# Kernel optimization log

Hardware: AMD Instinct MI355X
Metric: run time of the kernel (lower is better)

The kernel has to match this reference:

```python
import jax, jax.numpy as jnp
import numpy as np

B, T, D = 4, 8192, 1024
BLOCKS, TOPK, MACRO, SLOTS = 64, 16, 4, 64
RMS_EPS = 1.1920929e-07  # torch.finfo(float32).eps, F.rms_norm default


def setup_inputs() -> dict:
    key = jax.random.key(0)
    ks = jax.random.split(key, 7)
    return {
        "prev_hidden": jax.random.normal(ks[0], (B, T, D), jnp.float32),
        "prev_nll": jax.random.uniform(ks[1], (B, T), jnp.float32),
        "query": jax.random.normal(ks[2], (SLOTS, D), jnp.float32) * 0.02,
        "W_sum": jax.random.normal(ks[3], (D, 2 * D), jnp.float32) / np.sqrt(2 * D),
        "W_k": jax.random.normal(ks[4], (D, D), jnp.float32) / np.sqrt(D),
        "W_v": jax.random.normal(ks[5], (D, D), jnp.float32) / np.sqrt(D),
        "W_o": jax.random.normal(ks[6], (D, D), jnp.float32) / np.sqrt(D),
    }


def _rms_norm(x):
    return x * jax.lax.rsqrt(jnp.mean(x * x, axis=-1, keepdims=True) + RMS_EPS)


def _zscore(x):
    m = x.mean(axis=1, keepdims=True)
    s = jnp.maximum(x.std(axis=1, keepdims=True), 1e-6)  # unbiased=False
    return (x - m) / s


def reference(prev_hidden, prev_nll, query, W_sum, W_k, W_v, W_o):
    b, t, d = prev_hidden.shape
    # --- micro segments: equal blocks (t divisible by BLOCKS -> linspace edges exact)
    L = t // BLOCKS
    seg = prev_hidden.reshape(b, BLOCKS, L, d)
    seg_mean = seg.mean(axis=2)          # [B, BLOCKS, D]
    seg_last = seg[:, :, -1, :]          # [B, BLOCKS, D]
    hid_score = jnp.linalg.norm(seg_mean, axis=-1)            # [B, BLOCKS]
    sur_score = prev_nll.reshape(b, BLOCKS, L).mean(axis=-1)  # [B, BLOCKS]
    scores = _zscore(hid_score) + _zscore(sur_score)          # utility_source='both'
    idx = jnp.sort(jax.lax.top_k(scores, TOPK)[1], axis=-1)   # [B, TOPK]
    gmean = jnp.take_along_axis(seg_mean, idx[:, :, None], axis=1)
    glast = jnp.take_along_axis(seg_last, idx[:, :, None], axis=1)
    micro = jnp.concatenate([gmean, glast], axis=-1)          # [B, TOPK, 2D]
    # --- hierarchical: macro segments + global
    Lm = t // MACRO
    mseg = prev_hidden.reshape(b, MACRO, Lm, d)
    macro = jnp.concatenate([mseg.mean(axis=2), mseg[:, :, -1, :]], axis=-1)
    glob = jnp.concatenate([prev_hidden.mean(axis=1), prev_hidden[:, -1, :]], axis=-1)[:, None, :]
    feats = jnp.concatenate([micro, macro, glob], axis=1)     # [B, S=21, 2D]
    summaries = _rms_norm(jnp.einsum('bsf,df->bsd', feats, W_sum))
    # --- cross-attention of learned prefix queries over sources
    keys = jnp.einsum('bsd,ed->bse', summaries, W_k)
    vals = jnp.einsum('bsd,ed->bse', summaries, W_v)
    logits = jnp.einsum('qd,bsd->bqs', query, keys) / jnp.sqrt(jnp.float32(d))
    attn = jax.nn.softmax(logits.astype(jnp.float32), axis=-1).astype(summaries.dtype)
    prefix = jnp.einsum('bqs,bse->bqe', attn, vals)
    return jnp.einsum('bqe,oe->bqo', prefix, W_o)
```

## Files before the change

kernel.cpp:

```cpp
#include <hip/hip_runtime.h>
#include <stdint.h>
#include <stddef.h>

#define B_ 4
#define T_ 8192
#define D_ 1024
#define NBLK 64
#define SEGL 128
#define TOPK_ 16
#define NS 21
#define MPAD 96
#define RMS_EPS_ 1.1920929e-07f

typedef float f32x4 __attribute__((ext_vector_type(4)));
typedef __bf16 bf16x8 __attribute__((ext_vector_type(8)));
typedef unsigned short us8 __attribute__((ext_vector_type(8)));

__device__ __forceinline__ unsigned short f2bf(float f) {
    union { float f; unsigned int u; } v; v.f = f;
    unsigned int r = v.u + 0x7FFFu + ((v.u >> 16) & 1u);
    return (unsigned short)(r >> 16);
}
__device__ __forceinline__ float4 ld4(const float* p) { return *(const float4*)p; }

__global__ __launch_bounds__(512) void seg_stats(
        const float* __restrict__ ph, const float* __restrict__ nll,
        float* __restrict__ seg_mean, float* __restrict__ hid, float* __restrict__ sur) {
    int g = blockIdx.x; int b = g >> 6; int blk = g & 63;
    int tid = threadIdx.x; int half = tid >> 8; int c = tid & 255;
    const float* base = ph + ((size_t)b * T_ + blk * SEGL + half * 64) * D_ + 4 * c;
    float ax = 0.f, ay = 0.f, az = 0.f, aw = 0.f;
    #pragma unroll 8
    for (int r = 0; r < 64; r++) {
        float4 v = ld4(base + (size_t)r * D_);
        ax += v.x; ay += v.y; az += v.z; aw += v.w;
    }
    __shared__ float4 tmp[256];
    __shared__ float red[256];
    __shared__ float nl[128];
    if (tid < 128) nl[tid] = nll[b * T_ + blk * SEGL + tid];
    if (half) { float4 t; t.x = ax; t.y = ay; t.z = az; t.w = aw; tmp[c] = t; }
    __syncthreads();
    if (!half) {
        float4 t2 = tmp[c];
        float mx = (ax + t2.x) * (1.f/128.f), my = (ay + t2.y) * (1.f/128.f);
        float mz = (az + t2.z) * (1.f/128.f), mw = (aw + t2.w) * (1.f/128.f);
        float4 m; m.x = mx; m.y = my; m.z = mz; m.w = mw;
        *(float4*)(seg_mean + (size_t)g * D_ + 4 * c) = m;
        red[c] = mx*mx + my*my + mz*mz + mw*mw;
    }
    __syncthreads();
    for (int s2 = 128; s2 > 0; s2 >>= 1) { if (tid < s2) red[tid] += red[tid + s2]; __syncthreads(); }
    for (int s2 = 64;  s2 > 0; s2 >>= 1) { if (tid < s2) nl[tid]  += nl[tid + s2];  __syncthreads(); }
    if (tid == 0) { hid[g] = sqrtf(red[0]); sur[g] = nl[0] * (1.f/128.f); }
}

__global__ __launch_bounds__(64) void score_topk(
        const float* __restrict__ hid, const float* __restrict__ sur, int* __restrict__ idx) {
    int b = blockIdx.x; int l = threadIdx.x;
    float h = hid[b * NBLK + l];
    float s = sur[b * NBLK + l];
    float mh = h; for (int o = 32; o; o >>= 1) mh += __shfl_xor(mh, o); mh *= (1.f/64.f);
    float dh = h - mh; float vh = dh * dh;
    for (int o = 32; o; o >>= 1) vh += __shfl_xor(vh, o); vh *= (1.f/64.f);
    float sh = fmaxf(sqrtf(vh), 1e-6f);
    float ms = s; for (int o = 32; o; o >>= 1) ms += __shfl_xor(ms, o); ms *= (1.f/64.f);
    float ds = s - ms; float vs = ds * ds;
    for (int o = 32; o; o >>= 1) vs += __shfl_xor(vs, o); vs *= (1.f/64.f);
    float ss = fmaxf(sqrtf(vs), 1e-6f);
    float z = dh / sh + ds / ss;
    __shared__ float sc[64];
    sc[l] = z;
    __syncthreads();
    int rank = 0;
    for (int j = 0; j < 64; j++) {
        float oj = sc[j];
        rank += (oj > z) || (oj == z && j < l);
    }
    bool sel = rank < TOPK_;
    unsigned long long mask = __ballot(sel);
    int pos = __popcll(mask & ((1ull << l) - 1ull));
    if (sel) idx[b * TOPK_ + pos] = l;
}

__global__ __launch_bounds__(256) void feats_build(
        const float* __restrict__ ph, const float* __restrict__ seg_mean,
        const int* __restrict__ idx, unsigned short* __restrict__ feats) {
    int r = blockIdx.x; int t = threadIdx.x;
    unsigned short* row0 = feats + (size_t)r * 2048 + 4 * t;
    unsigned short* row1 = row0 + 1024;
    if (r >= B_ * NS) {
        ushort4 z; z.x = z.y = z.z = z.w = 0;
        *(ushort4*)row0 = z; *(ushort4*)row1 = z;
        return;
    }
    int b = r / NS, s = r % NS;
    float mx = 0, my = 0, mz = 0, mw = 0;
    int lastrow;
    if (s < 16) {
        int blk = idx[b * TOPK_ + s];
        float4 v = ld4(seg_mean + (size_t)(b * NBLK + blk) * D_ + 4 * t);
        mx = v.x; my = v.y; mz = v.z; mw = v.w;
        lastrow = blk * SEGL + SEGL - 1;
    } else if (s < 20) {
        int m = s - 16;
        for (int j = 0; j < 16; j++) {
            float4 v = ld4(seg_mean + (size_t)(b * NBLK + m * 16 + j) * D_ + 4 * t);
            mx += v.x; my += v.y; mz += v.z; mw += v.w;
        }
        mx *= (1.f/16.f); my *= (1.f/16.f); mz *= (1.f/16.f); mw *= (1.f/16.f);
        lastrow = m * 2048 + 2047;
    } else {
        for (int j = 0; j < 64; j++) {
            float4 v = ld4(seg_mean + (size_t)(b * NBLK + j) * D_ + 4 * t);
            mx += v.x; my += v.y; mz += v.z; mw += v.w;
        }
        mx *= (1.f/64.f); my *= (1.f/64.f); mz *= (1.f/64.f); mw *= (1.f/64.f);
        lastrow = T_ - 1;
    }
    float4 lv = ld4(ph + ((size_t)b * T_ + lastrow) * D_ + 4 * t);
    ushort4 hm; hm.x = f2bf(mx); hm.y = f2bf(my); hm.z = f2bf(mz); hm.w = f2bf(mw);
    ushort4 hl; hl.x = f2bf(lv.x); hl.y = f2bf(lv.y); hl.z = f2bf(lv.z); hl.w = f2bf(lv.w);
    *(ushort4*)row0 = hm;
    *(ushort4*)row1 = hl;
}

template<int K>
__global__ __launch_bounds__(256) void gemm_bt2(
        const unsigned short* __restrict__ A, const float* __restrict__ Bw,
        float* __restrict__ Cf, unsigned short* __restrict__ Cb) {
    constexpr int KW = K / 4;
    constexpr int NSTEP = KW / 32;
    int n0 = blockIdx.x * 16;
    int m0 = blockIdx.y * 48;
    int tid = threadIdx.x, wave = tid >> 6, lane = tid & 63;
    int quad = lane >> 4, l16 = lane & 15;
    int kbase = wave * KW;

    f32x4 acc[3];
    #pragma unroll
    for (int i = 0; i < 3; i++) acc[i] = (f32x4){0.f, 0.f, 0.f, 0.f};

    const float* bp = Bw + (size_t)(n0 + l16) * K + kbase + quad * 8;
    const unsigned short* ap = A + (size_t)(m0 + l16) * K + kbase + quad * 8;

    #pragma unroll 4
    for (int s = 0; s < NSTEP; s++) {
        float4 b0 = ld4(bp + s * 32);
        float4 b1 = ld4(bp + s * 32 + 4);
        us8 braw;
        braw[0] = f2bf(b0.x); braw[1] = f2bf(b0.y); braw[2] = f2bf(b0.z); braw[3] = f2bf(b0.w);
        braw[4] = f2bf(b1.x); braw[5] = f2bf(b1.y); braw[6] = f2bf(b1.z); braw[7] = f2bf(b1.w);
        bf16x8 bf = __builtin_bit_cast(bf16x8, braw);
        #pragma unroll
        for (int mi = 0; mi < 3; mi++) {
            us8 araw = *(const us8*)(ap + (size_t)mi * 16 * K + s * 32);
            bf16x8 af = __builtin_bit_cast(bf16x8, araw);
            acc[mi] = __builtin_amdgcn_mfma_f32_16x16x32_bf16(af, bf, acc[mi], 0, 0, 0);
        }
    }

    __shared__ float part[4][3][16][16];
    #pragma unroll
    for (int mi = 0; mi < 3; mi++)
        #pragma unroll
        for (int r = 0; r < 4; r++)
            part[wave][mi][quad * 4 + r][l16] = acc[mi][r];
    __syncthreads();
    for (int o = tid; o < 768; o += 256) {
        int mi = o >> 8; int rr = (o >> 4) & 15; int cc = o & 15;
        float v = part[0][mi][rr][cc] + part[1][mi][rr][cc]
                + part[2][mi][rr][cc] + part[3][mi][rr][cc];
        int row = m0 + mi * 16 + rr; int col = n0 + cc;
        Cf[(size_t)row * 1024 + col] = v;
        Cb[(size_t)row * 1024 + col] = f2bf(v);
    }
}

__global__ __launch_bounds__(256) void rmsnorm_rows(
        const float* __restrict__ x, unsigned short* __restrict__ y) {
    int r = blockIdx.x; int t = threadIdx.x;
    float4 v = ld4(x + (size_t)r * D_ + 4 * t);
    __shared__ float red[256];
    red[t] = v.x*v.x + v.y*v.y + v.z*v.z + v.w*v.w;
    __syncthreads();
    for (int s2 = 128; s2 > 0; s2 >>= 1) { if (t < s2) red[t] += red[t + s2]; __syncthreads(); }
    float scale = rsqrtf(red[0] * (1.f/1024.f) + RMS_EPS_);
    ushort4 h;
    h.x = f2bf(v.x * scale); h.y = f2bf(v.y * scale);
    h.z = f2bf(v.z * scale); h.w = f2bf(v.w * scale);
    *(ushort4*)(y + (size_t)r * D_ + 4 * t) = h;
}

__global__ __launch_bounds__(256) void attn_out(
        const float* __restrict__ query, const float* __restrict__ keys,
        const float* __restrict__ valsO, float* __restrict__ out) {
    int g = blockIdx.x; int b = g >> 6; int q = g & 63;
    int tid = threadIdx.x, wave = tid >> 6, lane = tid & 63;
    __shared__ float attnw[24];
    const float* qrow = query + (size_t)q * D_ + lane * 16;
    float4 qv0 = ld4(qrow), qv1 = ld4(qrow + 4), qv2 = ld4(qrow + 8), qv3 = ld4(qrow + 12);
    for (int s = wave; s < NS; s += 4) {
        const float* krow = keys + (size_t)(b * NS + s) * D_ + lane * 16;
        float4 k0 = ld4(krow), k1 = ld4(krow + 4), k2 = ld4(krow + 8), k3 = ld4(krow + 12);
        float a = qv0.x*k0.x + qv0.y*k0.y + qv0.z*k0.z + qv0.w*k0.w
                + qv1.x*k1.x + qv1.y*k1.y + qv1.z*k1.z + qv1.w*k1.w
                + qv2.x*k2.x + qv2.y*k2.y + qv2.z*k2.z + qv2.w*k2.w
                + qv3.x*k3.x + qv3.y*k3.y + qv3.z*k3.z + qv3.w*k3.w;
        for (int o = 32; o; o >>= 1) a += __shfl_xor(a, o);
        if (lane == 0) attnw[s] = a * 0.03125f;
    }
    __syncthreads();
    if (tid == 0) {
        float mx = -1e30f;
        for (int s = 0; s < NS; s++) mx = fmaxf(mx, attnw[s]);
        float sum = 0.f;
        for (int s = 0; s < NS; s++) { float e = expf(attnw[s] - mx); attnw[s] = e; sum += e; }
        float inv = 1.f / sum;
        for (int s = 0; s < NS; s++) attnw[s] *= inv;
    }
    __syncthreads();
    float ax = 0, ay = 0, az = 0, aw = 0;
    #pragma unroll
    for (int s = 0; s < NS; s++) {
        float w = attnw[s];
        float4 v = ld4(valsO + (size_t)(b * NS + s) * D_ + 4 * tid);
        ax += w * v.x; ay += w * v.y; az += w * v.z; aw += w * v.w;
    }
    float4 o4; o4.x = ax; o4.y = ay; o4.z = az; o4.w = aw;
    *(float4*)(out + (size_t)g * D_ + 4 * tid) = o4;
}

extern "C" void kernel_launch(void* const* d_in, const int* in_sizes, int n_in,
                              void* d_out, int out_size, void* d_ws, size_t ws_size,
                              hipStream_t stream) {
    (void)in_sizes; (void)n_in; (void)out_size; (void)ws_size;
    const float* ph    = (const float*)d_in[0];
    const float* nll   = (const float*)d_in[1];
    const float* query = (const float*)d_in[2];
    const float* W_sum = (const float*)d_in[3];
    const float* W_k   = (const float*)d_in[4];
    const float* W_v   = (const float*)d_in[5];
    const float* W_o   = (const float*)d_in[6];
    float* out = (float*)d_out;

    char* ws = (char*)d_ws;
    float*          seg_mean = (float*)(ws + 0);
    float*          hid      = (float*)(ws + 1048576);
    float*          sur      = (float*)(ws + 1049600);
    int*            idx      = (int*)  (ws + 1050624);
    unsigned short* feats    = (unsigned short*)(ws + 1050880);
    float*          presum_f = (float*)(ws + 1444096);
    unsigned short* presum_b = (unsigned short*)(ws + 1837312);
    unsigned short* summ_b   = (unsigned short*)(ws + 2033920);
    float*          keys_f   = (float*)(ws + 2230528);
    unsigned short* keys_b   = (unsigned short*)(ws + 2623744);
    float*          vals_f   = (float*)(ws + 2820352);
    unsigned short* vals_b   = (unsigned short*)(ws + 3213568);
    float*          valsO_f  = (float*)(ws + 3410176);
    unsigned short* valsO_b  = (unsigned short*)(ws + 3803392);

    seg_stats<<<B_ * NBLK, 512, 0, stream>>>(ph, nll, seg_mean, hid, sur);
    score_topk<<<B_, 64, 0, stream>>>(hid, sur, idx);
    feats_build<<<MPAD, 256, 0, stream>>>(ph, seg_mean, idx, feats);
    gemm_bt2<2048><<<dim3(64, 2), 256, 0, stream>>>(feats, W_sum, presum_f, presum_b);
    rmsnorm_rows<<<MPAD, 256, 0, stream>>>(presum_f, summ_b);
    gemm_bt2<1024><<<dim3(64, 2), 256, 0, stream>>>(summ_b, W_k, keys_f, keys_b);
    gemm_bt2<1024><<<dim3(64, 2), 256, 0, stream>>>(summ_b, W_v, vals_f, vals_b);
    gemm_bt2<1024><<<dim3(64, 2), 256, 0, stream>>>(vals_b, W_o, valsO_f, valsO_b);
    attn_out<<<B_ * NBLK, 256, 0, stream>>>(query, keys_f, valsO_f, out);
}
```

Before: 261.5 us.

## Fuse top-k into feats build, RMSnorm into GEMM, batch K/V projections

Folds the score/top-k kernel into feats_build, so each block recomputes the z-scores and ranks for its batch. The RMS sum of squares now comes from the W_sum GEMM epilogue via atomics, and the scale is applied while loading A in the next GEMM, which removes the rmsnorm kernel. The W_k and W_v GEMMs become a single launch that uses blockIdx.y to pick the weight. The GEMM changes from 4 to 8 waves with all 96 rows per block, and unused bf16/fp32 outputs are dropped. This removes several launches and intermediate buffers, at the cost of a memset, atomics, redundant top-k work per block, and fp32 A loads with on-the-fly conversion.

```diff
diff --git a/kernel.cpp b/kernel.cpp
--- a/kernel.cpp
+++ b/kernel.cpp
@@ -55,50 +55,53 @@
     if (tid == 0) { hid[g] = sqrtf(red[0]); sur[g] = nl[0] * (1.f/128.f); }
 }
 
-__global__ __launch_bounds__(64) void score_topk(
-        const float* __restrict__ hid, const float* __restrict__ sur, int* __restrict__ idx) {
-    int b = blockIdx.x; int l = threadIdx.x;
-    float h = hid[b * NBLK + l];
-    float s = sur[b * NBLK + l];
-    float mh = h; for (int o = 32; o; o >>= 1) mh += __shfl_xor(mh, o); mh *= (1.f/64.f);
-    float dh = h - mh; float vh = dh * dh;
-    for (int o = 32; o; o >>= 1) vh += __shfl_xor(vh, o); vh *= (1.f/64.f);
-    float sh = fmaxf(sqrtf(vh), 1e-6f);
-    float ms = s; for (int o = 32; o; o >>= 1) ms += __shfl_xor(ms, o); ms *= (1.f/64.f);
-    float ds = s - ms; float vs = ds * ds;
-    for (int o = 32; o; o >>= 1) vs += __shfl_xor(vs, o); vs *= (1.f/64.f);
-    float ss = fmaxf(sqrtf(vs), 1e-6f);
-    float z = dh / sh + ds / ss;
-    __shared__ float sc[64];
-    sc[l] = z;
-    __syncthreads();
-    int rank = 0;
-    for (int j = 0; j < 64; j++) {
-        float oj = sc[j];
-        rank += (oj > z) || (oj == z && j < l);
-    }
-    bool sel = rank < TOPK_;
-    unsigned long long mask = __ballot(sel);
-    int pos = __popcll(mask & ((1ull << l) - 1ull));
-    if (sel) idx[b * TOPK_ + pos] = l;
-}
-
 __global__ __launch_bounds__(256) void feats_build(
         const float* __restrict__ ph, const float* __restrict__ seg_mean,
-        const int* __restrict__ idx, unsigned short* __restrict__ feats) {
+        const float* __restrict__ hid, const float* __restrict__ sur,
+        unsigned short* __restrict__ feats) {
     int r = blockIdx.x; int t = threadIdx.x;
     unsigned short* row0 = feats + (size_t)r * 2048 + 4 * t;
     unsigned short* row1 = row0 + 1024;
     if (r >= B_ * NS) {
-        ushort4 z; z.x = z.y = z.z = z.w = 0;
-        *(ushort4*)row0 = z; *(ushort4*)row1 = z;
+        ushort4 z4; z4.x = z4.y = z4.z = z4.w = 0;
+        *(ushort4*)row0 = z4; *(ushort4*)row1 = z4;
         return;
     }
     int b = r / NS, s = r % NS;
+    __shared__ float sc[64];
+    __shared__ int sidx[16];
+    if (t < 64) {
+        float h = hid[b * NBLK + t];
+        float ss0 = sur[b * NBLK + t];
+        float mh = h; for (int o = 32; o; o >>= 1) mh += __shfl_xor(mh, o); mh *= (1.f/64.f);
+        float dh = h - mh; float vh = dh * dh;
+        for (int o = 32; o; o >>= 1) vh += __shfl_xor(vh, o); vh *= (1.f/64.f);
+        float sh = fmaxf(sqrtf(vh), 1e-6f);
+        float ms = ss0; for (int o = 32; o; o >>= 1) ms += __shfl_xor(ms, o); ms *= (1.f/64.f);
+        float ds = ss0 - ms; float vs = ds * ds;
+        for (int o = 32; o; o >>= 1) vs += __shfl_xor(vs, o); vs *= (1.f/64.f);
+        float ssd = fmaxf(sqrtf(vs), 1e-6f);
+        sc[t] = dh / sh + ds / ssd;
+    }
+    __syncthreads();
+    if (t < 64) {
+        float z = sc[t];
+        int rank = 0;
+        for (int j = 0; j < 64; j++) {
+            float oj = sc[j];
+            rank += (oj > z) || (oj == z && j < t);
+        }
+        bool sel = rank < TOPK_;
+        unsigned long long mask = __ballot(sel);
+        int pos = __popcll(mask & ((1ull << t) - 1ull));
+        if (sel) sidx[pos] = t;
+    }
+    __syncthreads();
+
     float mx = 0, my = 0, mz = 0, mw = 0;
     int lastrow;
     if (s < 16) {
-        int blk = idx[b * TOPK_ + s];
+        int blk = sidx[s];
         float4 v = ld4(seg_mean + (size_t)(b * NBLK + blk) * D_ + 4 * t);
         mx = v.x; my = v.y; mz = v.z; mw = v.w;
         lastrow = blk * SEGL + SEGL - 1;
@@ -125,24 +128,36 @@
     *(ushort4*)row1 = hl;
 }
 
-template<int K>
-__global__ __launch_bounds__(256) void gemm_bt2(
-        const unsigned short* __restrict__ A, const float* __restrict__ Bw,
-        float* __restrict__ Cf, unsigned short* __restrict__ Cb) {
-    constexpr int KW = K / 4;
+template<int K, int MODE>
+__global__ __launch_bounds__(512) void gemm_v3(
+        const void* __restrict__ Av,
+        const float* __restrict__ B0, const float* __restrict__ B1,
+        float* __restrict__ C0f, unsigned short* __restrict__ C0b,
+        float* __restrict__ C1f, unsigned short* __restrict__ C1b,
+        float* __restrict__ sumsq) {
+    constexpr int KW = K / 8;
     constexpr int NSTEP = KW / 32;
+    const float* Bw = (MODE == 2 && blockIdx.y) ? B1 : B0;
+    float* Cf          = (MODE == 2 && blockIdx.y) ? C1f : C0f;
+    unsigned short* Cb = (MODE == 2 && blockIdx.y) ? C1b : C0b;
+
     int n0 = blockIdx.x * 16;
-    int m0 = blockIdx.y * 48;
     int tid = threadIdx.x, wave = tid >> 6, lane = tid & 63;
     int quad = lane >> 4, l16 = lane & 15;
     int kbase = wave * KW;
 
-    f32x4 acc[3];
-    #pragma unroll
-    for (int i = 0; i < 3; i++) acc[i] = (f32x4){0.f, 0.f, 0.f, 0.f};
+    f32x4 acc[6];
+    #pragma unroll
+    for (int i = 0; i < 6; i++) acc[i] = (f32x4){0.f, 0.f, 0.f, 0.f};
+
+    float scl[6];
+    if (MODE == 2) {
+        #pragma unroll
+        for (int mi = 0; mi < 6; mi++)
+            scl[mi] = rsqrtf(sumsq[mi * 16 + l16] * (1.f/1024.f) + RMS_EPS_);
+    }
 
     const float* bp = Bw + (size_t)(n0 + l16) * K + kbase + quad * 8;
-    const unsigned short* ap = A + (size_t)(m0 + l16) * K + kbase + quad * 8;
 
     #pragma unroll 4
     for (int s = 0; s < NSTEP; s++) {
@@ -151,45 +166,52 @@
         us8 braw;
         braw[0] = f2bf(b0.x); braw[1] = f2bf(b0.y); braw[2] = f2bf(b0.z); braw[3] = f2bf(b0.w);
         braw[4] = f2bf(b1.x); braw[5] = f2bf(b1.y); braw[6] = f2bf(b1.z); braw[7] = f2bf(b1.w);
-        bf16x8 bf = __builtin_bit_cast(bf16x8, braw);
-        #pragma unroll
-        for (int mi = 0; mi < 3; mi++) {
-            us8 araw = *(const us8*)(ap + (size_t)mi * 16 * K + s * 32);
-            bf16x8 af = __builtin_bit_cast(bf16x8, araw);
-            acc[mi] = __builtin_amdgcn_mfma_f32_16x16x32_bf16(af, bf, acc[mi], 0, 0, 0);
-        }
-    }
-
-    __shared__ float part[4][3][16][16];
-    #pragma unroll
-    for (int mi = 0; mi < 3; mi++)
+        bf16x8 bfr = __builtin_bit_cast(bf16x8, braw);
+        #pragma unroll
+        for (int mi = 0; mi < 6; mi++) {
+            bf16x8 af;
+            if (MODE == 2) {
+                const float* apf = (const float*)Av + (size_t)(mi * 16 + l16) * K + kbase + quad * 8 + s * 32;
+                float4 a0 = ld4(apf), a1 = ld4(apf + 4);
+                us8 ar;
+                ar[0] = f2bf(a0.x * scl[mi]); ar[1] = f2bf(a0.y * scl[mi]);
+                ar[2] = f2bf(a0.z * scl[mi]); ar[3] = f2bf(a0.w * scl[mi]);
+                ar[4] = f2bf(a1.x * scl[mi]); ar[5] = f2bf(a1.y * scl[mi]);
+                ar[6] = f2bf(a1.z * scl[mi]); ar[7] = f2bf(a1.w * scl[mi]);
+                af = __builtin_bit_cast(bf16x8, ar);
+            } else {
+                af = __builtin_bit_cast(bf16x8,
+                    *(const us8*)((const unsigned short*)Av + (size_t)(mi * 16 + l16) * K + kbase + quad * 8 + s * 32));
+            }
+            acc[mi] = __builtin_amdgcn_mfma_f32_16x16x32_bf16(af, bfr, acc[mi], 0, 0, 0);
+        }
+    }
+
+    __shared__ float part[8][6][16][16];
+    #pragma unroll
+    for (int mi = 0; mi < 6; mi++)
         #pragma unroll
         for (int r = 0; r < 4; r++)
             part[wave][mi][quad * 4 + r][l16] = acc[mi][r];
     __syncthreads();
-    for (int o = tid; o < 768; o += 256) {
-        int mi = o >> 8; int rr = (o >> 4) & 15; int cc = o & 15;
-        float v = part[0][mi][rr][cc] + part[1][mi][rr][cc]
-                + part[2][mi][rr][cc] + part[3][mi][rr][cc];
-        int row = m0 + mi * 16 + rr; int col = n0 + cc;
-        Cf[(size_t)row * 1024 + col] = v;
-        Cb[(size_t)row * 1024 + col] = f2bf(v);
-    }
-}
-
-__global__ __launch_bounds__(256) void rmsnorm_rows(
-        const float* __restrict__ x, unsigned short* __restrict__ y) {
-    int r = blockIdx.x; int t = threadIdx.x;
-    float4 v = ld4(x + (size_t)r * D_ + 4 * t);
-    __shared__ float red[256];
-    red[t] = v.x*v.x + v.y*v.y + v.z*v.z + v.w*v.w;
-    __syncthreads();
-    for (int s2 = 128; s2 > 0; s2 >>= 1) { if (t < s2) red[t] += red[t + s2]; __syncthreads(); }
-    float scale = rsqrtf(red[0] * (1.f/1024.f) + RMS_EPS_);
-    ushort4 h;
-    h.x = f2bf(v.x * scale); h.y = f2bf(v.y * scale);
-    h.z = f2bf(v.z * scale); h.w = f2bf(v.w * scale);
-    *(ushort4*)(y + (size_t)r * D_ + 4 * t) = h;
+
+    #pragma unroll
+    for (int j = 0; j < 3; j++) {
+        int o = tid + j * 512;
+        int mi = o >> 8, rr = (o >> 4) & 15, cc = o & 15;
+        float v = 0.f;
+        #pragma unroll
+        for (int w = 0; w < 8; w++) v += part[w][mi][rr][cc];
+        int row = mi * 16 + rr, col = n0 + cc;
+        if (MODE == 1) {
+            float v2 = v * v;
+            #pragma unroll
+            for (int off = 1; off < 16; off <<= 1) v2 += __shfl_xor(v2, off);
+            if ((tid & 15) == 0) atomicAdd(&sumsq[row], v2);
+        }
+        if (Cf) Cf[(size_t)row * 1024 + col] = v;
+        if (Cb) Cb[(size_t)row * 1024 + col] = f2bf(v);
+    }
 }
 
 __global__ __launch_bounds__(256) void attn_out(
@@ -248,25 +270,21 @@
     float*          seg_mean = (float*)(ws + 0);
     float*          hid      = (float*)(ws + 1048576);
     float*          sur      = (float*)(ws + 1049600);
-    int*            idx      = (int*)  (ws + 1050624);
-    unsigned short* feats    = (unsigned short*)(ws + 1050880);
-    float*          presum_f = (float*)(ws + 1444096);
-    unsigned short* presum_b = (unsigned short*)(ws + 1837312);
-    unsigned short* summ_b   = (unsigned short*)(ws + 2033920);
-    float*          keys_f   = (float*)(ws + 2230528);
-    unsigned short* keys_b   = (unsigned short*)(ws + 2623744);
-    float*          vals_f   = (float*)(ws + 2820352);
-    unsigned short* vals_b   = (unsigned short*)(ws + 3213568);
-    float*          valsO_f  = (float*)(ws + 3410176);
-    unsigned short* valsO_b  = (unsigned short*)(ws + 3803392);
-
+    float*          sumsq    = (float*)(ws + 1050624);
+    unsigned short* feats    = (unsigned short*)(ws + 1051136);
+    float*          presum_f = (float*)(ws + 1444352);
+    float*          keys_f   = (float*)(ws + 1837568);
+    unsigned short* vals_b   = (unsigned short*)(ws + 2230784);
+    float*          valsO_f  = (float*)(ws + 2427392);
+
+    hipMemsetAsync(sumsq, 0, MPAD * sizeof(float), stream);
     seg_stats<<<B_ * NBLK, 512, 0, stream>>>(ph, nll, seg_mean, hid, sur);
-    score_topk<<<B_, 64, 0, stream>>>(hid, sur, idx);
-    feats_build<<<MPAD, 256, 0, stream>>>(ph, seg_mean, idx, feats);
-    gemm_bt2<2048><<<dim3(64, 2), 256, 0, stream>>>(feats, W_sum, presum_f, presum_b);
-    rmsnorm_rows<<<MPAD, 256, 0, stream>>>(presum_f, summ_b);
-    gemm_bt2<1024><<<dim3(64, 2), 256, 0, stream>>>(summ_b, W_k, keys_f, keys_b);
-    gemm_bt2<1024><<<dim3(64, 2), 256, 0, stream>>>(summ_b, W_v, vals_f, vals_b);
-    gemm_bt2<1024><<<dim3(64, 2), 256, 0, stream>>>(vals_b, W_o, valsO_f, valsO_b);
+    feats_build<<<MPAD, 256, 0, stream>>>(ph, seg_mean, hid, sur, feats);
+    gemm_v3<2048, 1><<<dim3(64, 1), 512, 0, stream>>>(
+        feats, W_sum, nullptr, presum_f, nullptr, nullptr, nullptr, sumsq);
+    gemm_v3<1024, 2><<<dim3(64, 2), 512, 0, stream>>>(
+        presum_f, W_k, W_v, keys_f, nullptr, nullptr, vals_b, sumsq);
+    gemm_v3<1024, 0><<<dim3(64, 1), 512, 0, stream>>>(
+        vals_b, W_o, nullptr, valsO_f, nullptr, nullptr, nullptr, nullptr);
     attn_out<<<B_ * NBLK, 256, 0, stream>>>(query, keys_f, valsO_f, out);
 }
```

Measured after the change: 272.7 us. +4.3%, slower.
